# Performance work log

Hardware: AMD Instinct MI355X
Metric: run time of the kernel (lower is better)

## Reference

```python
import jax, jax.numpy as jnp
import numpy as np
import math

B, S, F, R = 16, 2048, 512, 4
EPS = 1e-5

def setup_inputs() -> dict:
    key = jax.random.key(0)
    ks = jax.random.split(key, 8)
    s = 1.0 / math.sqrt(S)
    return {
        "x": jax.random.normal(ks[0], (B, S, F), dtype=jnp.float32),
        "Wq": jax.random.uniform(ks[1], (R, S), jnp.float32, -s, s),
        "bq": jnp.zeros((R,), jnp.float32),
        "Wk": jax.random.uniform(ks[2], (R, S), jnp.float32, -s, s),
        "bk": jnp.zeros((R,), jnp.float32),
        "Wv": jax.random.uniform(ks[3], (S, S), jnp.float32, -s, s),
        "bv": jnp.zeros((S,), jnp.float32),
        "ln_w": jnp.ones((S, F), jnp.float32),
        "ln_b": jnp.zeros((S, F), jnp.float32),
        "alpha": jnp.asarray(0.1, jnp.float32),
        "beta": jnp.asarray(0.1, jnp.float32),
    }

def reference(x, Wq, bq, Wk, bk, Wv, bv, ln_w, ln_b, alpha, beta):
    # LayerNorm over last two dims [S, F]
    mu = jnp.mean(x, axis=(1, 2), keepdims=True)
    var = jnp.mean(jnp.square(x - mu), axis=(1, 2), keepdims=True)
    x_norm = (x - mu) * jax.lax.rsqrt(var + EPS) * ln_w + ln_b
    x_t = jnp.swapaxes(x_norm, 1, 2)  # [B, F, S]
    Q = jnp.einsum('bfs,rs->bfr', x_t, Wq) + bq  # [B, F, R]
    K = jnp.einsum('bfs,rs->bfr', x_t, Wk) + bk  # [B, F, R]
    A = jnp.einsum('bfr,bgr->bfg', Q, K) / math.sqrt(R)  # [B, F, F]
    A = jax.nn.softmax(A, axis=-1)
    V = jnp.einsum('bfs,ts->bft', x_t, Wv) + bv  # [B, F, S]
    out = jnp.einsum('bfg,bgs->bfs', A, V)  # [B, F, S]
    # dropout in eval mode = identity
    out = x_t + alpha * out + V + beta * V
    return jnp.swapaxes(out, 1, 2)  # [B, S, F]
```

## Files before the change

kernel.cpp:

```cpp
#include <hip/hip_runtime.h>
#include <hip/hip_bf16.h>

#define NB 16
#define SS 2048
#define FF 512

typedef __bf16 bf16_t;
typedef __bf16 bf16x8 __attribute__((ext_vector_type(8)));
typedef __bf16 bf16x4 __attribute__((ext_vector_type(4)));
typedef float  f32x4  __attribute__((ext_vector_type(4)));

__global__ __launch_bounds__(256) void stats_kernel(const float* __restrict__ x,
                                                    float* __restrict__ partials) {
    const int b = blockIdx.y;
    const float* xb = x + ((size_t)b << 20) + (size_t)blockIdx.x * 16384;
    float s = 0.0f, ss = 0.0f;
#pragma unroll
    for (int i = 0; i < 16; ++i) {
        const float4 v = *(const float4*)&xb[(threadIdx.x + i * 256) * 4];
        s  += v.x + v.y + v.z + v.w;
        ss += v.x * v.x + v.y * v.y + v.z * v.z + v.w * v.w;
    }
#pragma unroll
    for (int off = 32; off > 0; off >>= 1) {
        s  += __shfl_down(s, off);
        ss += __shfl_down(ss, off);
    }
    __shared__ float ps[4], pss[4];
    const int w = threadIdx.x >> 6, lane = threadIdx.x & 63;
    if (lane == 0) { ps[w] = s; pss[w] = ss; }
    __syncthreads();
    if (threadIdx.x == 0) {
        partials[b * 64 + blockIdx.x]        = ps[0] + ps[1] + ps[2] + ps[3];
        partials[1024 + b * 64 + blockIdx.x] = pss[0] + pss[1] + pss[2] + pss[3];
    }
}

__global__ __launch_bounds__(256) void finalize_stats(const float* __restrict__ partials,
                                                      float* __restrict__ musig) {
    const int tid = threadIdx.x;
    const int b = tid >> 4, i = tid & 15;
    float s = 0.f, ss = 0.f;
#pragma unroll
    for (int j = 0; j < 4; ++j) {
        s  += partials[b * 64 + i * 4 + j];
        ss += partials[1024 + b * 64 + i * 4 + j];
    }
#pragma unroll
    for (int off = 8; off > 0; off >>= 1) {
        s  += __shfl_xor(s, off);
        ss += __shfl_xor(ss, off);
    }
    if (i == 0) {
        const float inv_n = 1.0f / 1048576.0f;
        const float mu  = s * inv_n;
        const float var = ss * inv_n - mu * mu;
        musig[b]      = mu;
        musig[16 + b] = rsqrtf(var + 1e-5f);
    }
}

__global__ __launch_bounds__(256) void ynorm_kernel(const float* __restrict__ x,
                                                    const float* __restrict__ lw,
                                                    const float* __restrict__ lb,
                                                    const float* __restrict__ musig,
                                                    bf16_t* __restrict__ Y) {
    __shared__ bf16_t t[32][33];
    const int b = blockIdx.z;
    const int f0 = blockIdx.x * 32, s0 = blockIdx.y * 32;
    const float mu = musig[b], rs = musig[16 + b];
    const int c = threadIdx.x & 31, rb = threadIdx.x >> 5;
#pragma unroll
    for (int i = 0; i < 4; ++i) {
        const int s_loc = rb + i * 8;
        const size_t idx = (size_t)(s0 + s_loc) * FF + f0 + c;
        const float yv = (x[((size_t)b << 20) + idx] - mu) * rs * lw[idx] + lb[idx];
        t[s_loc][c] = (bf16_t)yv;
    }
    __syncthreads();
#pragma unroll
    for (int i = 0; i < 4; ++i) {
        const int f_loc = rb + i * 8;
        Y[((size_t)b << 20) + (size_t)(f0 + f_loc) * SS + s0 + c] = t[c][f_loc];
    }
}

__global__ __launch_bounds__(256) void cast_wv(const float* __restrict__ Wv,
                                               bf16_t* __restrict__ Wvb) {
    const size_t i = ((size_t)blockIdx.x * 256 + threadIdx.x) * 4;
    const float4 v = *(const float4*)&Wv[i];
    bf16x4 o;
    o[0] = (bf16_t)v.x; o[1] = (bf16_t)v.y; o[2] = (bf16_t)v.z; o[3] = (bf16_t)v.w;
    *(bf16x4*)&Wvb[i] = o;
}

__global__ __launch_bounds__(256) void qk_kernel(const bf16_t* __restrict__ Y,
                                                 const float* __restrict__ Wq,
                                                 const float* __restrict__ bq,
                                                 const float* __restrict__ Wk,
                                                 const float* __restrict__ bk,
                                                 float* __restrict__ Qo,
                                                 float* __restrict__ Ko) {
    const int w = threadIdx.x >> 6, lane = threadIdx.x & 63;
    const int row = blockIdx.x * 4 + w;
    const bf16_t* y = Y + (size_t)row * SS;
    float qa[4] = {0.f, 0.f, 0.f, 0.f}, ka[4] = {0.f, 0.f, 0.f, 0.f};
#pragma unroll
    for (int c = 0; c < 4; ++c) {
        const int s = c * 512 + lane * 8;
        const bf16x8 yv = *(const bf16x8*)&y[s];
        float yf[8];
#pragma unroll
        for (int j = 0; j < 8; ++j) yf[j] = (float)yv[j];
#pragma unroll
        for (int r = 0; r < 4; ++r) {
            const float4 a0 = *(const float4*)&Wq[r * SS + s];
            const float4 a1 = *(const float4*)&Wq[r * SS + s + 4];
            const float4 c0 = *(const float4*)&Wk[r * SS + s];
            const float4 c1 = *(const float4*)&Wk[r * SS + s + 4];
            qa[r] += yf[0]*a0.x + yf[1]*a0.y + yf[2]*a0.z + yf[3]*a0.w
                   + yf[4]*a1.x + yf[5]*a1.y + yf[6]*a1.z + yf[7]*a1.w;
            ka[r] += yf[0]*c0.x + yf[1]*c0.y + yf[2]*c0.z + yf[3]*c0.w
                   + yf[4]*c1.x + yf[5]*c1.y + yf[6]*c1.z + yf[7]*c1.w;
        }
    }
#pragma unroll
    for (int off = 32; off > 0; off >>= 1) {
#pragma unroll
        for (int r = 0; r < 4; ++r) {
            qa[r] += __shfl_down(qa[r], off);
            ka[r] += __shfl_down(ka[r], off);
        }
    }
    if (lane == 0) {
#pragma unroll
        for (int r = 0; r < 4; ++r) {
            Qo[(size_t)row * 4 + r] = qa[r] + bq[r];
            Ko[(size_t)row * 4 + r] = ka[r] + bk[r];
        }
    }
}

__global__ __launch_bounds__(256) void softmax_kernel(const float* __restrict__ Qo,
                                                      const float* __restrict__ Ko,
                                                      bf16_t* __restrict__ Aout) {
    const int w = threadIdx.x >> 6, lane = threadIdx.x & 63;
    const int row = blockIdx.x * 4 + w;
    const int b = row >> 9;
    const float4 q = *(const float4*)&Qo[(size_t)row * 4];
    const float* kb = Ko + (size_t)b * FF * 4;
    float sc[8];
#pragma unroll
    for (int j = 0; j < 8; ++j) {
        const float4 kv = *(const float4*)&kb[(lane * 8 + j) * 4];
        sc[j] = (q.x*kv.x + q.y*kv.y + q.z*kv.z + q.w*kv.w) * 0.5f;
    }
    float mx = sc[0];
#pragma unroll
    for (int j = 1; j < 8; ++j) mx = fmaxf(mx, sc[j]);
#pragma unroll
    for (int off = 32; off > 0; off >>= 1) mx = fmaxf(mx, __shfl_xor(mx, off));
    float sum = 0.f;
#pragma unroll
    for (int j = 0; j < 8; ++j) { sc[j] = __expf(sc[j] - mx); sum += sc[j]; }
#pragma unroll
    for (int off = 32; off > 0; off >>= 1) sum += __shfl_xor(sum, off);
    const float inv = 1.0f / sum;
    bf16x8 o;
#pragma unroll
    for (int j = 0; j < 8; ++j) o[j] = (bf16_t)(sc[j] * inv);
    *(bf16x8*)&Aout[(size_t)row * FF + lane * 8] = o;
}

template<bool FUSE>
__global__ __launch_bounds__(512, 2) void gemm_nt_8phase(
        const bf16_t* __restrict__ Abase, long long strideA, int lda,
        const bf16_t* __restrict__ Bbase, long long strideB, int ldb,
        bf16_t* __restrict__ Cbase, long long strideC, int ldc,
        int NTILES, const float* __restrict__ bias_m,
        const float* __restrict__ xp, const float* __restrict__ lwp,
        const float* __restrict__ lbp, const float* __restrict__ musig,
        const float* __restrict__ alphap, const float* __restrict__ betap,
        float* __restrict__ outp) {
    __shared__ __align__(16) bf16_t As[2][16384];
    __shared__ __align__(16) bf16_t Bs[2][16384];
    const int tid = threadIdx.x;
    const int w = tid >> 6, lane = tid & 63;

    const int nchunk = gridDim.x >> 3;
    const int wgid = (blockIdx.x & 7) * nchunk + (blockIdx.x >> 3);
    const int bz = wgid >> 4;
    const int rem = wgid & 15;
    const int m0 = (rem & 7) * 256, n0 = (rem >> 3) * 256;

    const bf16_t* A = Abase + (size_t)bz * (size_t)strideA;
    const bf16_t* B = Bbase + (size_t)bz * (size_t)strideB;
    bf16_t* C = Cbase + (size_t)bz * (size_t)strideC;
    const int wm = w >> 2, wn = w & 3;

    const int rr0 = (w * 2 + 0) * 16 + (lane >> 2);
    const int rr1 = (w * 2 + 1) * 16 + (lane >> 2);
    const int sw0 = ((lane & 3) ^ ((rr0 >> 1) & 3)) * 8;
    const int sw1 = ((lane & 3) ^ ((rr1 >> 1) & 3)) * 8;
    const bf16_t* gA0 = A + (size_t)(m0 + rr0) * lda + sw0;
    const bf16_t* gA1 = A + (size_t)(m0 + rr1) * lda + sw1;
    const bf16_t* gB0 = B + (size_t)(n0 + rr0) * ldb + sw0;
    const bf16_t* gB1 = B + (size_t)(n0 + rr1) * ldb + sw1;
    const int d0 = (w * 2 + 0) * 512;
    const int d1 = (w * 2 + 1) * 512;

#define STA(bi, h, ko) do {                                                          \
    __builtin_amdgcn_global_load_lds(                                                \
        (const __attribute__((address_space(1))) unsigned int*)(gA0 + (ko) + (h)*32),\
        (__attribute__((address_space(3))) unsigned int*)&As[bi][(h)*8192 + d0], 16, 0, 0); \
    __builtin_amdgcn_global_load_lds(                                                \
        (const __attribute__((address_space(1))) unsigned int*)(gA1 + (ko) + (h)*32),\
        (__attribute__((address_space(3))) unsigned int*)&As[bi][(h)*8192 + d1], 16, 0, 0); \
} while (0)
#define STB(bi, h, ko) do {                                                          \
    __builtin_amdgcn_global_load_lds(                                                \
        (const __attribute__((address_space(1))) unsigned int*)(gB0 + (ko) + (h)*32),\
        (__attribute__((address_space(3))) unsigned int*)&Bs[bi][(h)*8192 + d0], 16, 0, 0); \
    __builtin_amdgcn_global_load_lds(                                                \
        (const __attribute__((address_space(1))) unsigned int*)(gB1 + (ko) + (h)*32),\
        (__attribute__((address_space(3))) unsigned int*)&Bs[bi][(h)*8192 + d1], 16, 0, 0); \
} while (0)

    const int cs = lane >> 4;
    int offA[2][8], offB[2][4];
#pragma unroll
    for (int kk = 0; kk < 2; ++kk) {
#pragma unroll
        for (int mt = 0; mt < 8; ++mt) {
            const int r = wm * 128 + mt * 16 + (lane & 15);
            offA[kk][mt] = kk * 8192 + r * 32 + ((cs ^ ((r >> 1) & 3)) << 3);
        }
#pragma unroll
        for (int nt = 0; nt < 4; ++nt) {
            const int r = wn * 64 + nt * 16 + (lane & 15);
            offB[kk][nt] = kk * 8192 + r * 32 + ((cs ^ ((r >> 1) & 3)) << 3);
        }
    }

#define DS_A(kk, mh) do { _Pragma("unroll")                                   \
    for (int i = 0; i < 4; ++i) af[i] = *(const bf16x8*)&as[offA[kk][(mh)*4 + i]]; } while (0)
#define DS_B(kk) do { _Pragma("unroll")                                       \
    for (int i = 0; i < 4; ++i) bfr[i] = *(const bf16x8*)&bs[offB[kk][i]]; } while (0)
#define MFMA16(mh) do { _Pragma("unroll")                                     \
    for (int i = 0; i < 4; ++i) { _Pragma("unroll")                           \
        for (int nt = 0; nt < 4; ++nt)                                        \
            acc[(mh)*4 + i][nt] = __builtin_amdgcn_mfma_f32_16x16x32_bf16(    \
                af[i], bfr[nt], acc[(mh)*4 + i][nt], 0, 0, 0); } } while (0)
#define VM4   asm volatile("s_waitcnt vmcnt(4)" ::: "memory")
#define HBAR  __builtin_amdgcn_s_barrier()
#define LGKM0 do { asm volatile("s_waitcnt lgkmcnt(0)" ::: "memory");         \
                   __builtin_amdgcn_sched_barrier(0); } while (0)
#define SBAR  __builtin_amdgcn_sched_barrier(0)
#define PRIO1 __builtin_amdgcn_s_setprio(1)
#define PRIO0 __builtin_amdgcn_s_setprio(0)

    f32x4 acc[8][4] = {};
    const int mask = NTILES - 1;

    STA(0, 0, 0); STB(0, 0, 0); STA(0, 1, 0); STB(0, 1, 0);
    VM4; HBAR;

    for (int t = 0; t < NTILES; ++t) {
        const int oth = (t & 1) ^ 1;
        const int ko = ((t + 1) & mask) * 64;
        const bf16_t* as = As[t & 1];
        const bf16_t* bs = Bs[t & 1];
        bf16x8 af[4], bfr[4];
        DS_A(0, 0); DS_B(0); SBAR;
        STA(oth, 0, ko); SBAR;
        HBAR;
        LGKM0;
        PRIO1; MFMA16(0); PRIO0; SBAR;
        HBAR;
        DS_A(0, 1); SBAR;
        STB(oth, 0, ko); SBAR;
        VM4;
        HBAR;
        LGKM0;
        PRIO1; MFMA16(1); PRIO0; SBAR;
        HBAR;
        DS_A(1, 0); DS_B(1); SBAR;
        STA(oth, 1, ko); SBAR;
        HBAR;
        LGKM0;
        PRIO1; MFMA16(0); PRIO0; SBAR;
        HBAR;
        DS_A(1, 1); SBAR;
        STB(oth, 1, ko); SBAR;
        VM4;
        HBAR;
        LGKM0;
        PRIO1; MFMA16(1); PRIO0; SBAR;
        HBAR;
    }
#undef STA
#undef STB
#undef DS_A
#undef DS_B
#undef MFMA16
#undef VM4
#undef HBAR
#undef LGKM0
#undef SBAR
#undef PRIO1
#undef PRIO0

    if constexpr (!FUSE) {
#pragma unroll
        for (int mt = 0; mt < 8; ++mt) {
#pragma unroll
            for (int r = 0; r < 4; ++r) {
                const int row = m0 + wm * 128 + mt * 16 + ((lane >> 4) << 2) + r;
                const float bm = bias_m ? bias_m[row] : 0.0f;
#pragma unroll
                for (int nt = 0; nt < 4; ++nt) {
                    const int col = n0 + wn * 64 + nt * 16 + (lane & 15);
                    C[(size_t)row * ldc + col] = (bf16_t)(acc[mt][nt][r] + bm);
                }
            }
        }
    } else {
        asm volatile("s_waitcnt vmcnt(0)" ::: "memory");
        __syncthreads();
        float* lsc = (float*)&As[0][0];
        const float mu = musig[bz], rs = musig[16 + bz];
        const float alpha = alphap[0];
        const float onepb = 1.0f + betap[0];
        const float* xb = xp + ((size_t)bz << 20);
        float* ob = outp + ((size_t)bz << 20);
        const int lrow = wm * 16 + ((lane >> 4) << 2);
        const int lcol = wn * 64 + (lane & 15);
        const int gr = tid >> 4;
        const int gc = (tid & 15) * 16;
        for (int mt = 0; mt < 8; ++mt) {
#pragma unroll
            for (int r = 0; r < 4; ++r)
#pragma unroll
                for (int nt = 0; nt < 4; ++nt)
                    lsc[(lrow + r) * 256 + lcol + nt * 16] = acc[mt][nt][r];
            __syncthreads();
            const int grow = m0 + (gr >> 4) * 128 + mt * 16 + (gr & 15);
            const size_t idx = (size_t)grow * FF + n0 + gc;
#pragma unroll
            for (int j = 0; j < 4; ++j) {
                const float4 av = *(const float4*)&lsc[gr * 256 + gc + j * 4];
                const float4 xv = *(const float4*)&xb[idx + j * 4];
                const float4 wv = *(const float4*)&lwp[idx + j * 4];
                const float4 bv4 = *(const float4*)&lbp[idx + j * 4];
                const bf16x4 vv = *(const bf16x4*)&A[idx + j * 4];
                float4 o;
                o.x = (xv.x - mu) * rs * wv.x + bv4.x + alpha * av.x + onepb * (float)vv[0];
                o.y = (xv.y - mu) * rs * wv.y + bv4.y + alpha * av.y + onepb * (float)vv[1];
                o.z = (xv.z - mu) * rs * wv.z + bv4.z + alpha * av.z + onepb * (float)vv[2];
                o.w = (xv.w - mu) * rs * wv.w + bv4.w + alpha * av.w + onepb * (float)vv[3];
                *(float4*)&ob[idx + j * 4] = o;
            }
            __syncthreads();
        }
    }
}

extern "C" void kernel_launch(void* const* d_in, const int* in_sizes, int n_in,
                              void* d_out, int out_size, void* d_ws, size_t ws_size,
                              hipStream_t stream) {
    const float* x   = (const float*)d_in[0];
    const float* Wq  = (const float*)d_in[1];
    const float* bq  = (const float*)d_in[2];
    const float* Wk  = (const float*)d_in[3];
    const float* bk  = (const float*)d_in[4];
    const float* Wv  = (const float*)d_in[5];
    const float* bv  = (const float*)d_in[6];
    const float* lw  = (const float*)d_in[7];
    const float* lb  = (const float*)d_in[8];
    const float* alp = (const float*)d_in[9];
    const float* bet = (const float*)d_in[10];
    float* out = (float*)d_out;

    char* ws = (char*)d_ws;
    float*  musig = (float*)(ws + 128);
    float*  Qo    = (float*)(ws + 256);
    float*  Ko    = (float*)(ws + 256 + 131072);
    bf16_t* Wvb   = (bf16_t*)(ws + 262400);
    bf16_t* Asm   = (bf16_t*)(ws + 8651008);
    float*  partials = (float*)(ws + 8651008);
    bf16_t* Vt    = (bf16_t*)(ws + 17039616);
    bf16_t* Y     = (bf16_t*)(ws + 50594048);

    stats_kernel<<<dim3(64, 16), 256, 0, stream>>>(x, partials);
    finalize_stats<<<1, 256, 0, stream>>>(partials, musig);
    cast_wv<<<4096, 256, 0, stream>>>(Wv, Wvb);
    ynorm_kernel<<<dim3(16, 64, 16), 256, 0, stream>>>(x, lw, lb, musig, Y);
    qk_kernel<<<2048, 256, 0, stream>>>(Y, Wq, bq, Wk, bk, Qo, Ko);
    softmax_kernel<<<2048, 256, 0, stream>>>(Qo, Ko, Asm);
    gemm_nt_8phase<false><<<256, 512, 0, stream>>>(
        Wvb, 0, SS, Y, 1 << 20, SS, Vt, 1 << 20, FF, 32, bv,
        nullptr, nullptr, nullptr, nullptr, nullptr, nullptr, nullptr);
    gemm_nt_8phase<true><<<256, 512, 0, stream>>>(
        Vt, 1 << 20, FF, Asm, FF * FF, FF, nullptr, 0, FF, 8, nullptr,
        x, lw, lb, musig, alp, bet, out);
}
```

Measured before the change: 197.0 us.

## Double-buffer GEMM register fragments, drop half the barriers, vectorize ynorm transpose

The GEMM main loop now keeps two sets of A/B register fragments. LDS reads for the next phase, including the first phase of the next tile from the other buffer, are issued before the current MFMAs. Partial lgkmcnt waits replace full drains, and the per-tile barrier count drops from eight to two, so LDS latency and barrier stalls should overlap with MFMA work. The ynorm transpose kernel switches to float4 loads and bf16x4 stores with a different LDS padding. The main risks are race hazards from fewer barriers when reading the other buffer, and higher register pressure under the 2-wave occupancy bound.

New measurement: 192.3 us. -2.4%, faster.

```diff
diff --git a/kernel.cpp b/kernel.cpp
--- a/kernel.cpp
+++ b/kernel.cpp
@@ -65,23 +65,31 @@
                                                     const float* __restrict__ lb,
                                                     const float* __restrict__ musig,
                                                     bf16_t* __restrict__ Y) {
-    __shared__ bf16_t t[32][33];
+    __shared__ bf16_t t[32][36];
     const int b = blockIdx.z;
     const int f0 = blockIdx.x * 32, s0 = blockIdx.y * 32;
     const float mu = musig[b], rs = musig[16 + b];
-    const int c = threadIdx.x & 31, rb = threadIdx.x >> 5;
-#pragma unroll
-    for (int i = 0; i < 4; ++i) {
-        const int s_loc = rb + i * 8;
-        const size_t idx = (size_t)(s0 + s_loc) * FF + f0 + c;
-        const float yv = (x[((size_t)b << 20) + idx] - mu) * rs * lw[idx] + lb[idx];
-        t[s_loc][c] = (bf16_t)yv;
+    const int tid = threadIdx.x;
+    {
+        const int s_loc = tid >> 3, c4 = (tid & 7) * 4;
+        const size_t idx = (size_t)(s0 + s_loc) * FF + f0 + c4;
+        const float4 xv = *(const float4*)&x[((size_t)b << 20) + idx];
+        const float4 wv = *(const float4*)&lw[idx];
+        const float4 bv = *(const float4*)&lb[idx];
+        t[s_loc][c4 + 0] = (bf16_t)((xv.x - mu) * rs * wv.x + bv.x);
+        t[s_loc][c4 + 1] = (bf16_t)((xv.y - mu) * rs * wv.y + bv.y);
+        t[s_loc][c4 + 2] = (bf16_t)((xv.z - mu) * rs * wv.z + bv.z);
+        t[s_loc][c4 + 3] = (bf16_t)((xv.w - mu) * rs * wv.w + bv.w);
     }
     __syncthreads();
-#pragma unroll
-    for (int i = 0; i < 4; ++i) {
-        const int f_loc = rb + i * 8;
-        Y[((size_t)b << 20) + (size_t)(f0 + f_loc) * SS + s0 + c] = t[c][f_loc];
+    {
+        const int f_loc = tid >> 3, s4 = (tid & 7) * 4;
+        bf16x4 o;
+        o[0] = t[s4 + 0][f_loc];
+        o[1] = t[s4 + 1][f_loc];
+        o[2] = t[s4 + 2][f_loc];
+        o[3] = t[s4 + 3][f_loc];
+        *(bf16x4*)&Y[((size_t)b << 20) + (size_t)(f0 + f_loc) * SS + s0 + s4] = o;
     }
 }
 
@@ -173,7 +181,7 @@
 }
 
 template<bool FUSE>
-__global__ __launch_bounds__(512, 2) void gemm_nt_8phase(
+__global__ __launch_bounds__(512, 2) void gemm_nt_pipe(
         const bf16_t* __restrict__ Abase, long long strideA, int lda,
         const bf16_t* __restrict__ Bbase, long long strideB, int ldb,
         bf16_t* __restrict__ Cbase, long long strideC, int ldc,
@@ -242,70 +250,65 @@
         }
     }
 
-#define DS_A(kk, mh) do { _Pragma("unroll")                                   \
-    for (int i = 0; i < 4; ++i) af[i] = *(const bf16x8*)&as[offA[kk][(mh)*4 + i]]; } while (0)
-#define DS_B(kk) do { _Pragma("unroll")                                       \
-    for (int i = 0; i < 4; ++i) bfr[i] = *(const bf16x8*)&bs[offB[kk][i]]; } while (0)
-#define MFMA16(mh) do { _Pragma("unroll")                                     \
+#define RD_A(dst, base, kk, mh) do { _Pragma("unroll")                        \
+    for (int i = 0; i < 4; ++i) dst[i] = *(const bf16x8*)&(base)[offA[kk][(mh)*4 + i]]; } while (0)
+#define RD_B(dst, base, kk) do { _Pragma("unroll")                            \
+    for (int i = 0; i < 4; ++i) dst[i] = *(const bf16x8*)&(base)[offB[kk][i]]; } while (0)
+#define MFMA16X(af, bfr, mh) do { _Pragma("unroll")                           \
     for (int i = 0; i < 4; ++i) { _Pragma("unroll")                           \
         for (int nt = 0; nt < 4; ++nt)                                        \
             acc[(mh)*4 + i][nt] = __builtin_amdgcn_mfma_f32_16x16x32_bf16(    \
                 af[i], bfr[nt], acc[(mh)*4 + i][nt], 0, 0, 0); } } while (0)
-#define VM4   asm volatile("s_waitcnt vmcnt(4)" ::: "memory")
+#define VMC(n) asm volatile("s_waitcnt vmcnt(" #n ")" ::: "memory")
 #define HBAR  __builtin_amdgcn_s_barrier()
-#define LGKM0 do { asm volatile("s_waitcnt lgkmcnt(0)" ::: "memory");         \
-                   __builtin_amdgcn_sched_barrier(0); } while (0)
+#define LGKM(n) do { asm volatile("s_waitcnt lgkmcnt(" #n ")" ::: "memory");  \
+                     __builtin_amdgcn_sched_barrier(0); } while (0)
 #define SBAR  __builtin_amdgcn_sched_barrier(0)
 #define PRIO1 __builtin_amdgcn_s_setprio(1)
 #define PRIO0 __builtin_amdgcn_s_setprio(0)
 
     f32x4 acc[8][4] = {};
+    bf16x8 afA[4], afB[4], bfrA[4], bfrB[4];
     const int mask = NTILES - 1;
 
     STA(0, 0, 0); STB(0, 0, 0); STA(0, 1, 0); STB(0, 1, 0);
-    VM4; HBAR;
+    VMC(4); HBAR;
+    RD_A(afA, As[0], 0, 0); RD_B(bfrA, Bs[0], 0);
 
     for (int t = 0; t < NTILES; ++t) {
-        const int oth = (t & 1) ^ 1;
+        const int cur = t & 1, oth = cur ^ 1;
         const int ko = ((t + 1) & mask) * 64;
-        const bf16_t* as = As[t & 1];
-        const bf16_t* bs = Bs[t & 1];
-        bf16x8 af[4], bfr[4];
-        DS_A(0, 0); DS_B(0); SBAR;
+        const bf16_t* as  = As[cur];
+        const bf16_t* bs  = Bs[cur];
+        const bf16_t* asn = As[oth];
+        const bf16_t* bsn = Bs[oth];
+        RD_A(afB, as, 0, 1); SBAR;
         STA(oth, 0, ko); SBAR;
-        HBAR;
-        LGKM0;
-        PRIO1; MFMA16(0); PRIO0; SBAR;
-        HBAR;
-        DS_A(0, 1); SBAR;
+        LGKM(4);
+        PRIO1; MFMA16X(afA, bfrA, 0); PRIO0; SBAR;
+        VMC(2); HBAR;
+        RD_A(afA, as, 1, 0); RD_B(bfrB, bs, 1); SBAR;
         STB(oth, 0, ko); SBAR;
-        VM4;
-        HBAR;
-        LGKM0;
-        PRIO1; MFMA16(1); PRIO0; SBAR;
-        HBAR;
-        DS_A(1, 0); DS_B(1); SBAR;
+        LGKM(8);
+        PRIO1; MFMA16X(afB, bfrA, 1); PRIO0; SBAR;
+        RD_A(afB, as, 1, 1); SBAR;
         STA(oth, 1, ko); SBAR;
-        HBAR;
-        LGKM0;
-        PRIO1; MFMA16(0); PRIO0; SBAR;
-        HBAR;
-        DS_A(1, 1); SBAR;
+        LGKM(4);
+        PRIO1; MFMA16X(afA, bfrB, 0); PRIO0; SBAR;
+        VMC(2); HBAR;
+        RD_A(afA, asn, 0, 0); RD_B(bfrA, bsn, 0); SBAR;
         STB(oth, 1, ko); SBAR;
-        VM4;
-        HBAR;
-        LGKM0;
-        PRIO1; MFMA16(1); PRIO0; SBAR;
-        HBAR;
+        LGKM(8);
+        PRIO1; MFMA16X(afB, bfrB, 1); PRIO0; SBAR;
     }
 #undef STA
 #undef STB
-#undef DS_A
-#undef DS_B
-#undef MFMA16
-#undef VM4
+#undef RD_A
+#undef RD_B
+#undef MFMA16X
+#undef VMC
 #undef HBAR
-#undef LGKM0
+#undef LGKM
 #undef SBAR
 #undef PRIO1
 #undef PRIO0
@@ -325,7 +328,7 @@
             }
         }
     } else {
-        asm volatile("s_waitcnt vmcnt(0)" ::: "memory");
+        asm volatile("s_waitcnt vmcnt(0) lgkmcnt(0)" ::: "memory");
         __syncthreads();
         float* lsc = (float*)&As[0][0];
         const float mu = musig[bz], rs = musig[16 + bz];
@@ -397,10 +400,10 @@
     ynorm_kernel<<<dim3(16, 64, 16), 256, 0, stream>>>(x, lw, lb, musig, Y);
     qk_kernel<<<2048, 256, 0, stream>>>(Y, Wq, bq, Wk, bk, Qo, Ko);
     softmax_kernel<<<2048, 256, 0, stream>>>(Qo, Ko, Asm);
-    gemm_nt_8phase<false><<<256, 512, 0, stream>>>(
+    gemm_nt_pipe<false><<<256, 512, 0, stream>>>(
         Wvb, 0, SS, Y, 1 << 20, SS, Vt, 1 << 20, FF, 32, bv,
         nullptr, nullptr, nullptr, nullptr, nullptr, nullptr, nullptr);
-    gemm_nt_8phase<true><<<256, 512, 0, stream>>>(
+    gemm_nt_pipe<true><<<256, 512, 0, stream>>>(
         Vt, 1 << 20, FF, Asm, FF * FF, FF, nullptr, 0, FF, 8, nullptr,
         x, lw, lb, musig, alp, bet, out);
 }
```
